# Kernel optimization log

Measured on AMD Instinct MI355X. Metric: run time of the kernel, lower is better.

## Reference

```python
import jax, jax.numpy as jnp
import numpy as np

B, S, DIM = 2, 2048, 2048
H, DH = 16, 128            # head_dim = dim // n_heads; decop_rot_dim == head_dim (required by the view)
LKV, LQ = 512, 1024        # latent kv / q compression dims


def setup_inputs() -> dict:
    key = jax.random.key(0)
    ks = jax.random.split(key, 12)
    w = lambda k, shape: jax.random.normal(k, shape, jnp.float32) * 0.02
    x = jax.random.normal(ks[0], (B, S, DIM), jnp.float32)
    # rotary table: angles[t, i] = t * 10000^(-2i/DH), complex passed as cos/sin pair
    inv_freq = 1.0 / (10000.0 ** (np.arange(0, DH, 2, dtype=np.float64) / DH))
    ang = np.outer(np.arange(S, dtype=np.float64), inv_freq)  # [S, DH/2]
    return {
        "x": x,
        "freq_cos": jnp.asarray(np.cos(ang), jnp.float32),
        "freq_sin": jnp.asarray(np.sin(ang), jnp.float32),
        "w_lq": w(ks[1], (LQ, DIM)),
        "w_lkv": w(ks[2], (LKV, DIM)),
        "w_q": w(ks[3], (H * DH, LQ)),
        "w_k": w(ks[4], (H * DH, LKV)),
        "w_v": w(ks[5], (H * DH, LKV)),
        "w_qr": w(ks[6], (H * DH, LQ)),
        "b_qr": w(ks[7], (H * DH,)),
        "w_kr": w(ks[8], (H * DH, DIM)),
        "b_kr": w(ks[9], (H * DH,)),
        "w_o": w(ks[10], (DIM, H * DH)),
        "b_o": w(ks[11], (DIM,)),
    }


def _rope(t, freq):
    # t: [B,S,H,DH]; freq: [S,DH/2] complex. Pairs (even,odd) along last dim rotated.
    b, s, h, d = t.shape
    tc = t.astype(jnp.float32).reshape(b, s, h, d // 2, 2)
    tc = jax.lax.complex(tc[..., 0], tc[..., 1]) * freq[None, :, None, :]
    return jnp.stack([jnp.real(tc), jnp.imag(tc)], axis=-1).reshape(b, s, h, d).astype(t.dtype)


def reference(x, freq_cos, freq_sin, w_lq, w_lkv, w_q, w_k, w_v, w_qr, b_qr, w_kr, b_kr, w_o, b_o):
    b, s, _ = x.shape
    freq = jax.lax.complex(freq_cos, freq_sin)          # [S, DH/2]
    cq = x @ w_lq.T                                      # [B,S,LQ]
    ckv = x @ w_lkv.T                                    # [B,S,LKV]
    q = (cq @ w_q.T).reshape(b, s, H, DH)
    qr = _rope((cq @ w_qr.T + b_qr).reshape(b, s, H, DH), freq)
    k = (ckv @ w_k.T).reshape(b, s, H, DH)
    kr = _rope((x @ w_kr.T + b_kr).reshape(b, s, H, DH), freq)
    v = (ckv @ w_v.T).reshape(b, s, H, DH)
    q = jnp.concatenate([q, qr], axis=-1)                # [B,S,H,2*DH]
    k = jnp.concatenate([k, kr], axis=-1)
    # note: scale uses sqrt(head_dim), NOT sqrt(2*head_dim), faithful to source
    scores = jnp.einsum('bqhd,bkhd->bhqk', q, k) / jnp.sqrt(jnp.float32(DH))
    att = jax.nn.softmax(scores.astype(jnp.float32), axis=-1).astype(q.dtype)
    out = jnp.einsum('bhqk,bkhd->bqhd', att, v).reshape(b, s, H * DH)
    return out @ w_o.T + b_o
```

## Files before the change

### kernel.cpp

```cpp
#include <hip/hip_runtime.h>
#include <hip/hip_bf16.h>


#define Bb 2
#define Ss 2048
#define DIMd 2048
#define Hh 16
#define DHd 128

typedef __hip_bfloat16 bf16;
typedef __attribute__((ext_vector_type(8))) short short8;
typedef __attribute__((ext_vector_type(4))) float floatx4;
typedef __attribute__((ext_vector_type(16))) float floatx16;
typedef __attribute__((ext_vector_type(2))) unsigned int uintx2;

#define MFMA(a, b, c) __builtin_amdgcn_mfma_f32_16x16x32_bf16((a), (b), (c), 0, 0, 0)
#define MFMA32(a, b, c) __builtin_amdgcn_mfma_f32_32x32x16_bf16((a), (b), (c), 0, 0, 0)

#define CEF (0.08838834764831845f * 1.4426950408889634f)

__device__ __forceinline__ void async16(const bf16* g, bf16* l) {
  __builtin_amdgcn_global_load_lds(
      (const __attribute__((address_space(1))) unsigned int*)g,
      (__attribute__((address_space(3))) unsigned int*)l, 16, 0, 0);
}

__global__ __launch_bounds__(256) void cvt_all(
    const float* x, const float* wlq, const float* wlkv, const float* wq,
    const float* wqr, const float* wk, const float* wv, const float* wkr,
    const float* wo, bf16* dx, bf16* dwlq, bf16* dwlkv, bf16* dwq, bf16* dwqr,
    bf16* dwk, bf16* dwv, bf16* dwkr, bf16* dwo) {
  long i = (long)blockIdx.x * 256 + threadIdx.x;
  const float* src;
  bf16* dst;
  long base;
  if (i < 2097152L)      { src = x;    dst = dx;    base = 0; }
  else if (i < 2621440L) { src = wlq;  dst = dwlq;  base = 2097152L; }
  else if (i < 2883584L) { src = wlkv; dst = dwlkv; base = 2621440L; }
  else if (i < 3407872L) { src = wq;   dst = dwq;   base = 2883584L; }
  else if (i < 3932160L) { src = wqr;  dst = dwqr;  base = 3407872L; }
  else if (i < 4194304L) { src = wk;   dst = dwk;   base = 3932160L; }
  else if (i < 4456448L) { src = wv;   dst = dwv;   base = 4194304L; }
  else if (i < 5505024L) { src = wkr;  dst = dwkr;  base = 4456448L; }
  else                   { src = wo;   dst = dwo;   base = 5505024L; }
  long j = i - base;
  float4 f = ((const float4*)src)[j];
  union { ushort4 u4; bf16 h[4]; } cv;
  cv.h[0] = __float2bfloat16(f.x);
  cv.h[1] = __float2bfloat16(f.y);
  cv.h[2] = __float2bfloat16(f.z);
  cv.h[3] = __float2bfloat16(f.w);
  ((ushort4*)dst)[j] = cv.u4;
}

template <int MODE>
__device__ __forceinline__ void gemm_body(const bf16* __restrict__ A,
                                          const bf16* __restrict__ Bw,
                                          const float* __restrict__ bias,
                                          void* __restrict__ Cout,
                                          void* __restrict__ Cout2,
                                          const float* __restrict__ fco,
                                          const float* __restrict__ fsi,
                                          int M, int N, int K, int lda) {
  extern __shared__ __align__(16) bf16 smem[];
  bf16* As = smem;
  bf16* Bs = smem + 8192;
  const int tid = threadIdx.x;
  const int lane = tid & 63;
  const int w = tid >> 6;
  const int wm = w & 1, wn = w >> 1;
  const int m0 = blockIdx.y * 128, n0 = blockIdx.x * 128;
  const int lr = lane & 15, lg = lane >> 4;

  floatx4 acc[4][4];
#pragma unroll
  for (int mi = 0; mi < 4; ++mi)
#pragma unroll
    for (int ni = 0; ni < 4; ++ni)
#pragma unroll
      for (int r = 0; r < 4; ++r) acc[mi][ni][r] = 0.f;

  for (int k0 = 0; k0 < K; k0 += 64) {
    __syncthreads();
#pragma unroll
    for (int i = 0; i < 4; ++i) {
      int c = i * 256 + tid;
      int row = c >> 3;
      int cg = (c & 7) ^ (row & 7);
      async16(A + (size_t)(m0 + row) * lda + k0 + cg * 8, As + (i * 256 + w * 64) * 8);
      async16(Bw + (size_t)(n0 + row) * K + k0 + cg * 8, Bs + (i * 256 + w * 64) * 8);
    }
    __syncthreads();

#pragma unroll
    for (int ks = 0; ks < 2; ++ks) {
      short8 af[4], bfr[4];
#pragma unroll
      for (int mi = 0; mi < 4; ++mi) {
        int row = wm * 64 + mi * 16 + lr;
        af[mi] = *(const short8*)&As[row * 64 + (((ks * 4 + lg) ^ (lr & 7)) * 8)];
      }
#pragma unroll
      for (int ni = 0; ni < 4; ++ni) {
        int row = wn * 64 + ni * 16 + lr;
        bfr[ni] = *(const short8*)&Bs[row * 64 + (((ks * 4 + lg) ^ (lr & 7)) * 8)];
      }
#pragma unroll
      for (int mi = 0; mi < 4; ++mi)
#pragma unroll
        for (int ni = 0; ni < 4; ++ni)
          acc[mi][ni] = MFMA(af[mi], bfr[ni], acc[mi][ni]);
    }
  }

  if (MODE == 5 && n0 >= 2048) {
    __syncthreads();
#pragma unroll
    for (int mi = 0; mi < 4; ++mi)
#pragma unroll
      for (int ni = 0; ni < 4; ++ni)
#pragma unroll
        for (int r = 0; r < 4; ++r) {
          int ml = wm * 64 + mi * 16 + lg * 4 + r;
          int nl = wn * 64 + ni * 16 + lr;
          smem[ml * 129 + nl] = __float2bfloat16(acc[mi][ni][r]);
        }
    __syncthreads();
    int bb = m0 >> 11, s0 = m0 & 2047;
    int hh = (n0 - 2048) >> 7;
    short* vbase = (short*)Cout2 + ((size_t)(bb * Hh + hh) * 128) * Ss;
#pragma unroll
    for (int pa = 0; pa < 8; ++pa) {
      int d = pa * 16 + (tid >> 4);
      int sc = (tid & 15) * 8;
      short8 v;
#pragma unroll
      for (int i = 0; i < 8; ++i) v[i] = *(const short*)&smem[(sc + i) * 129 + d];
      *(short8*)(vbase + (size_t)d * Ss + s0 + sc) = v;
    }
    return;
  }

#pragma unroll
  for (int mi = 0; mi < 4; ++mi)
#pragma unroll
    for (int ni = 0; ni < 4; ++ni)
#pragma unroll
      for (int r = 0; r < 4; ++r) {
        int m = m0 + wm * 64 + mi * 16 + lg * 4 + r;
        int n = n0 + wn * 64 + ni * 16 + lr;
        float v = acc[mi][ni][r];
        int bb = m >> 11, s = m & 2047;
        if (MODE == 3) {
          v += bias[n];
          ((float*)Cout)[(size_t)m * N + n] = v;
        } else if (MODE == 4) {
          if (n < 2048) {
            int hh = n >> 7, d = n & 127;
            ((bf16*)Cout)[((size_t)((bb * Hh + hh) * Ss + s)) * 256 + d] =
                __float2bfloat16(v * CEF);
          } else {
            int n2 = n - 2048;
            int hh = n2 >> 7, d = n2 & 127;
            v += bias[n2];
            float vp = __shfl_xor(v, 1, 64);
            float co = fco[s * 64 + (d >> 1)];
            float sn = fsi[s * 64 + (d >> 1)];
            v = (d & 1) ? (v * co + vp * sn) : (v * co - vp * sn);
            ((bf16*)Cout)[((size_t)((bb * Hh + hh) * Ss + s)) * 256 + 128 + d] =
                __float2bfloat16(v * CEF);
          }
        } else if (MODE == 5) {
          int hh = n >> 7, d = n & 127;
          ((bf16*)Cout)[((size_t)((bb * Hh + hh) * Ss + s)) * 256 + d] =
              __float2bfloat16(v);
        } else if (MODE == 6) {
          if (n < 1536) {
            ((bf16*)Cout)[(size_t)m * 1536 + n] = __float2bfloat16(v);
          } else {
            int n2 = n - 1536;
            int hh = n2 >> 7, d = n2 & 127;
            v += bias[n2];
            float vp = __shfl_xor(v, 1, 64);
            float co = fco[s * 64 + (d >> 1)];
            float sn = fsi[s * 64 + (d >> 1)];
            v = (d & 1) ? (v * co + vp * sn) : (v * co - vp * sn);
            ((bf16*)Cout2)[((size_t)((bb * Hh + hh) * Ss + s)) * 256 + 128 + d] =
                __float2bfloat16(v);
          }
        }
      }
}

template <int MODE>
__global__ __launch_bounds__(256, 4) void gemm_bt(const bf16* __restrict__ A,
                                                  const bf16* __restrict__ Bw,
                                                  const float* __restrict__ bias,
                                                  void* __restrict__ Cout,
                                                  void* __restrict__ Cout2,
                                                  const float* __restrict__ fco,
                                                  const float* __restrict__ fsi,
                                                  int M, int N, int K, int lda) {
  gemm_body<MODE>(A, Bw, bias, Cout, Cout2, fco, fsi, M, N, K, lda);
}

__global__ __launch_bounds__(256, 4) void gemm_qkv(const bf16* __restrict__ ccat,
                                                   const bf16* __restrict__ wqcat,
                                                   const bf16* __restrict__ wkvcat,
                                                   const float* __restrict__ bqr,
                                                   void* __restrict__ qcat,
                                                   void* __restrict__ kcat,
                                                   void* __restrict__ vt,
                                                   const float* __restrict__ fco,
                                                   const float* __restrict__ fsi) {
  if (blockIdx.z == 0)
    gemm_body<4>(ccat, wqcat, bqr, qcat, nullptr, fco, fsi, 4096, 4096, 1024, 1536);
  else
    gemm_body<5>(ccat + 1024, wkvcat, nullptr, kcat, vt, nullptr, nullptr, 4096, 4096, 512, 1536);
}

#define FA_STAGE(KSN, VSN, J)                                                    \
  {                                                                              \
    _Pragma("unroll") for (int i = 0; i < 4; ++i) {                              \
      int r = w * 8 + i * 2 + (lane >> 5);                                       \
      async16(Kb + (size_t)((J) + r) * 256 + (((lane & 31) ^ (r & 7)) * 8),      \
              KSN + (w * 8 + i * 2) * 256);                                      \
    }                                                                            \
    _Pragma("unroll") for (int i = 0; i < 2; ++i) {                              \
      int d = w * 32 + i * 16 + (lane >> 2);                                     \
      async16(Vb + (size_t)d * Ss + (J) + (((lane & 3) ^ ((d >> 1) & 3)) * 8),   \
              VSN + (w * 32 + i * 16) * 32);                                     \
    }                                                                            \
  }

#define FA_QKT(KP)                                                               \
  {                                                                              \
    _Pragma("unroll") for (int r = 0; r < 16; ++r) sf[r] = 0.f;                  \
    __builtin_amdgcn_s_setprio(1);                                               \
    _Pragma("unroll") for (int dt = 0; dt < 16; ++dt) {                          \
      short8 kf = *(const short8*)(KP[dt & 3] + (dt >> 2) * 64);                 \
      sf = MFMA32(kf, qf[dt], sf);                                               \
    }                                                                            \
    __builtin_amdgcn_s_setprio(0);                                               \
  }

#define FA_SM()                                                                  \
  {                                                                              \
    _Pragma("unroll") for (int rp = 0; rp < 8; ++rp) {                           \
      float p0 = exp2f(sf[2 * rp]);                                              \
      float p1 = exp2f(sf[2 * rp + 1]);                                          \
      l += p0 + p1;                                                              \
      bf16 b0 = __float2bfloat16(p0);                                            \
      bf16 b1 = __float2bfloat16(p1);                                            \
      pk[rp] = ((unsigned)*(const unsigned short*)&b1 << 16) |                   \
               *(const unsigned short*)&b0;                                      \
    }                                                                            \
  }

#define FA_PV(VQ)                                                                \
  {                                                                              \
    __builtin_amdgcn_s_setprio(1);                                               \
    _Pragma("unroll") for (int kb = 0; kb < 2; ++kb) {                           \
      uintx2 w02 = __builtin_amdgcn_permlane32_swap(pk[kb * 4 + 0],              \
                                                    pk[kb * 4 + 2], false, false); \
      uintx2 w13 = __builtin_amdgcn_permlane32_swap(pk[kb * 4 + 1],              \
                                                    pk[kb * 4 + 3], false, false); \
      union { unsigned u[4]; short8 s; } pa;                                     \
      pa.u[0] = w02.x; pa.u[1] = w13.x; pa.u[2] = w02.y; pa.u[3] = w13.y;        \
      _Pragma("unroll") for (int nb = 0; nb < 4; ++nb) {                         \
        short8 vf = *(const short8*)(VQ[kb] + nb * 1024);                        \
        oacc[nb] = MFMA32(pa.s, vf, oacc[nb]);                                   \
      }                                                                          \
    }                                                                            \
    __builtin_amdgcn_s_setprio(0);                                               \
  }

#define FA_BODY(VQpv, KPqk, KSst, VSst, Jst)                                     \
  FA_STAGE(KSst, VSst, Jst);                                                     \
  FA_PV(VQpv);                                                                   \
  asm volatile("s_waitcnt vmcnt(6)" ::: "memory");                               \
  __builtin_amdgcn_s_barrier();                                                  \
  FA_QKT(KPqk);                                                                  \
  FA_SM();

__global__ __launch_bounds__(256, 2) void flash_attn(const bf16* __restrict__ Q,
                                                     const bf16* __restrict__ Kc,
                                                     const bf16* __restrict__ Vt,
                                                     bf16* __restrict__ Oa) {
  __shared__ __align__(16) bf16 Ks0[32 * 256];
  __shared__ __align__(16) bf16 Ks1[32 * 256];
  __shared__ __align__(16) bf16 Ks2[32 * 256];
  __shared__ __align__(16) bf16 Vs0[128 * 32];
  __shared__ __align__(16) bf16 Vs1[128 * 32];
  __shared__ __align__(16) bf16 Vs2[128 * 32];

  const int lane = threadIdx.x & 63;
  const int w = threadIdx.x >> 6;
  const int m = lane & 31;
  const int hi = lane >> 5;
  const int bh = blockIdx.x;
  const int b = bh >> 4, h = bh & 15;
  const int q0 = blockIdx.y * 128 + w * 32;

  const bf16* Qb = Q + (size_t)bh * Ss * 256;
  const bf16* Kb = Kc + (size_t)bh * Ss * 256;
  const bf16* Vb = Vt + (size_t)bh * 128 * Ss;

  short8 qf[16];
  {
    const short* Qrow = (const short*)Qb + (size_t)(q0 + m) * 256 + hi * 8;
#pragma unroll
    for (int dt = 0; dt < 16; ++dt) qf[dt] = *(const short8*)(Qrow + dt * 16);
  }

  const int key = m & 7;
  const int vkey = (m >> 1) & 3;
  const short *kp0[4], *kp1[4], *kp2[4];
#pragma unroll
  for (int dl = 0; dl < 4; ++dl) {
    int off = m * 256 + (((2 * dl + hi) ^ key) * 8);
    kp0[dl] = (const short*)Ks0 + off;
    kp1[dl] = (const short*)Ks1 + off;
    kp2[dl] = (const short*)Ks2 + off;
  }
  const short *vq0[2], *vq1[2], *vq2[2];
#pragma unroll
  for (int kb = 0; kb < 2; ++kb) {
    int off = m * 32 + (((2 * kb + hi) ^ vkey) * 8);
    vq0[kb] = (const short*)Vs0 + off;
    vq1[kb] = (const short*)Vs1 + off;
    vq2[kb] = (const short*)Vs2 + off;
  }

  float l = 0.f;
  floatx16 sf;
  unsigned pk[8];
  floatx16 oacc[4];
#pragma unroll
  for (int nb = 0; nb < 4; ++nb)
#pragma unroll
    for (int r = 0; r < 16; ++r) oacc[nb][r] = 0.f;

  FA_STAGE(Ks0, Vs0, 0);
  FA_STAGE(Ks1, Vs1, 32);
  asm volatile("s_waitcnt vmcnt(6)" ::: "memory");
  __builtin_amdgcn_s_barrier();
  FA_QKT(kp0);
  FA_SM();

#pragma unroll 1
  for (int c = 0; c < 20; ++c) {
    const int j2 = (3 * c + 2) * 32;
    FA_BODY(vq0, kp1, Ks2, Vs2, j2);
    FA_BODY(vq1, kp2, Ks0, Vs0, j2 + 32);
    FA_BODY(vq2, kp0, Ks1, Vs1, j2 + 64);
  }
  FA_BODY(vq0, kp1, Ks2, Vs2, 62 * 32);
  FA_BODY(vq1, kp2, Ks0, Vs0, 63 * 32);
  FA_PV(vq2);
  asm volatile("s_waitcnt vmcnt(0)" ::: "memory");
  __builtin_amdgcn_s_barrier();
  FA_QKT(kp0);
  FA_SM();
  FA_PV(vq0);

  float lsum = l + __shfl_xor(l, 32, 64);
  float inv = 1.f / lsum;

#pragma unroll
  for (int r = 0; r < 16; ++r) {
    int qr = (r & 3) + 8 * (r >> 2) + 4 * hi;
    float invr = __shfl(inv, (lane & 32) + qr, 64);
    int s = q0 + qr;
#pragma unroll
    for (int nb = 0; nb < 4; ++nb) {
      int d = nb * 32 + m;
      Oa[((size_t)(b * Ss + s)) * (Hh * 128) + h * 128 + d] =
          __float2bfloat16(oacc[nb][r] * invr);
    }
  }
}

extern "C" void kernel_launch(void* const* d_in, const int* in_sizes, int n_in,
                              void* d_out, int out_size, void* d_ws, size_t ws_size,
                              hipStream_t stream) {
  const float* x    = (const float*)d_in[0];
  const float* fco  = (const float*)d_in[1];
  const float* fsi  = (const float*)d_in[2];
  const float* wlq  = (const float*)d_in[3];
  const float* wlkv = (const float*)d_in[4];
  const float* wq   = (const float*)d_in[5];
  const float* wk   = (const float*)d_in[6];
  const float* wv   = (const float*)d_in[7];
  const float* wqr  = (const float*)d_in[8];
  const float* bqr  = (const float*)d_in[9];
  const float* wkr  = (const float*)d_in[10];
  const float* bkr  = (const float*)d_in[11];
  const float* wo   = (const float*)d_in[12];
  const float* bo   = (const float*)d_in[13];

  char* ws = (char*)d_ws;
  size_t o = 0;
  bf16* x_b    = (bf16*)(ws + o); o += (size_t)Bb * Ss * DIMd * 2;
  bf16* wbig   = (bf16*)(ws + o); o += (size_t)3584 * 2048 * 2;
  bf16* wqcat  = (bf16*)(ws + o); o += (size_t)4096 * 1024 * 2;
  bf16* wkvcat = (bf16*)(ws + o); o += (size_t)4096 * 512 * 2;
  bf16* wo_b   = (bf16*)(ws + o); o += (size_t)2048 * 2048 * 2;
  bf16* ccat   = (bf16*)(ws + o); o += (size_t)4096 * 1536 * 2;
  bf16* qcat   = (bf16*)(ws + o); o += (size_t)Bb * Hh * Ss * 256 * 2;
  bf16* kcat   = (bf16*)(ws + o); o += (size_t)Bb * Hh * Ss * 256 * 2;
  bf16* vt     = (bf16*)(ws + o); o += (size_t)Bb * Hh * 128 * Ss * 2;
  bf16* attn   = (bf16*)(ws + o); o += (size_t)4096 * 2048 * 2;

  cvt_all<<<25600, 256, 0, stream>>>(
      x, wlq, wlkv, wq, wqr, wk, wv, wkr, wo,
      x_b,
      wbig,
      wbig + (size_t)1024 * 2048,
      wqcat,
      wqcat + (size_t)2048 * 1024,
      wkvcat,
      wkvcat + (size_t)2048 * 512,
      wbig + (size_t)1536 * 2048,
      wo_b);

  const int M = Bb * Ss;
  const int GEMM_LDS = 128 * 129 * 2;
  gemm_bt<6><<<dim3(28, 32), 256, GEMM_LDS, stream>>>(
      x_b, wbig, bkr, ccat, kcat, fco, fsi, M, 3584, 2048, 2048);
  gemm_qkv<<<dim3(32, 32, 2), 256, GEMM_LDS, stream>>>(
      ccat, wqcat, wkvcat, bqr, qcat, kcat, vt, fco, fsi);

  flash_attn<<<dim3(Bb * Hh, Ss / 128), 256, 0, stream>>>(qcat, kcat, vt, attn);

  gemm_bt<3><<<dim3(16, 32), 256, GEMM_LDS, stream>>>(
      attn, wo_b, bo, (float*)d_out, nullptr, nullptr, nullptr, M, 2048, 2048, 2048);
}
```

Baseline: 454.5 us.

## Add 256x256-tile double-buffered GEMM for latent and Q projections

Adds a new 512-thread GEMM kernel with 256x256 output tiles, 128KB of double-buffered LDS loaded asynchronously with XOR swizzling, and MFMA priority hints. It is used for the x→latent/kr projection and the Q/QR projection. The K/V projection is split back into its own launch of the old 128-tile kernel. The goal is more data reuse per tile and better overlap of loads with MFMA work. In exchange, occupancy drops, the latent GEMM grid becomes small (224 blocks), and the fused QKV launch turns into two launches.

```diff
diff --git a/kernel.cpp b/kernel.cpp
--- a/kernel.cpp
+++ b/kernel.cpp
@@ -154,7 +154,120 @@
         if (MODE == 3) {
           v += bias[n];
           ((float*)Cout)[(size_t)m * N + n] = v;
-        } else if (MODE == 4) {
+        } else if (MODE == 5) {
+          int hh = n >> 7, d = n & 127;
+          ((bf16*)Cout)[((size_t)((bb * Hh + hh) * Ss + s)) * 256 + d] =
+              __float2bfloat16(v);
+        }
+      }
+}
+
+template <int MODE>
+__global__ __launch_bounds__(256, 4) void gemm_bt(const bf16* __restrict__ A,
+                                                  const bf16* __restrict__ Bw,
+                                                  const float* __restrict__ bias,
+                                                  void* __restrict__ Cout,
+                                                  void* __restrict__ Cout2,
+                                                  const float* __restrict__ fco,
+                                                  const float* __restrict__ fsi,
+                                                  int M, int N, int K, int lda) {
+  gemm_body<MODE>(A, Bw, bias, Cout, Cout2, fco, fsi, M, N, K, lda);
+}
+
+#define G2_STAGE(BUF, TT)                                                      \
+  {                                                                            \
+    bf16* db = smem + (BUF) * 32768;                                           \
+    _Pragma("unroll") for (int i = 0; i < 4; ++i) {                            \
+      int c = i * 512 + tid;                                                   \
+      int row = c >> 3;                                                        \
+      int cg = (c & 7) ^ (row & 7);                                            \
+      async16(A + (size_t)(m0 + row) * lda + (TT) * 64 + cg * 8,               \
+              db + (i * 512 + w * 64) * 8);                                    \
+    }                                                                          \
+    _Pragma("unroll") for (int i = 0; i < 4; ++i) {                            \
+      int c = i * 512 + tid;                                                   \
+      int row = c >> 3;                                                        \
+      int cg = (c & 7) ^ (row & 7);                                            \
+      async16(Bw + (size_t)(n0 + row) * KTOT + (TT) * 64 + cg * 8,             \
+              db + 16384 + (i * 512 + w * 64) * 8);                            \
+    }                                                                          \
+  }
+
+#define G2_COMPUTE(BUF)                                                        \
+  {                                                                            \
+    const bf16* cb = smem + (BUF) * 32768;                                     \
+    _Pragma("unroll") for (int ks = 0; ks < 2; ++ks) {                         \
+      short8 af[8], bq[4];                                                     \
+      _Pragma("unroll") for (int mi = 0; mi < 8; ++mi) {                       \
+        int row = wm * 128 + mi * 16 + lr;                                     \
+        af[mi] = *(const short8*)&cb[row * 64 + (((ks * 4 + lg) ^ (lr & 7)) * 8)]; \
+      }                                                                        \
+      _Pragma("unroll") for (int ni = 0; ni < 4; ++ni) {                       \
+        int row = wn * 64 + ni * 16 + lr;                                      \
+        bq[ni] = *(const short8*)&cb[16384 + row * 64 +                        \
+                                     (((ks * 4 + lg) ^ (lr & 7)) * 8)];        \
+      }                                                                        \
+      __builtin_amdgcn_s_setprio(1);                                           \
+      _Pragma("unroll") for (int mi = 0; mi < 8; ++mi)                         \
+        _Pragma("unroll") for (int ni = 0; ni < 4; ++ni)                       \
+            acc[mi][ni] = MFMA(af[mi], bq[ni], acc[mi][ni]);                   \
+      __builtin_amdgcn_s_setprio(0);                                           \
+    }                                                                          \
+  }
+
+template <int MODE, int KTOT>
+__global__ __launch_bounds__(512, 2) void gemm256(const bf16* __restrict__ A,
+                                                  const bf16* __restrict__ Bw,
+                                                  const float* __restrict__ bias,
+                                                  void* __restrict__ Cout,
+                                                  void* __restrict__ Cout2,
+                                                  const float* __restrict__ fco,
+                                                  const float* __restrict__ fsi,
+                                                  int M, int N, int lda) {
+  extern __shared__ __align__(16) bf16 smem[];
+  constexpr int NT = KTOT / 64;
+  const int tid = threadIdx.x;
+  const int lane = tid & 63;
+  const int w = tid >> 6;
+  const int wm = w >> 2, wn = w & 3;
+  const int m0 = blockIdx.y * 256, n0 = blockIdx.x * 256;
+  const int lr = lane & 15, lg = lane >> 4;
+
+  floatx4 acc[8][4];
+#pragma unroll
+  for (int mi = 0; mi < 8; ++mi)
+#pragma unroll
+    for (int ni = 0; ni < 4; ++ni)
+#pragma unroll
+      for (int r = 0; r < 4; ++r) acc[mi][ni][r] = 0.f;
+
+  G2_STAGE(0, 0);
+  asm volatile("s_waitcnt vmcnt(0)" ::: "memory");
+  __builtin_amdgcn_s_barrier();
+
+#pragma unroll 1
+  for (int t = 0; t < NT; t += 2) {
+    G2_STAGE(1, t + 1);
+    G2_COMPUTE(0);
+    asm volatile("s_waitcnt vmcnt(0)" ::: "memory");
+    __builtin_amdgcn_s_barrier();
+    if (t + 2 < NT) G2_STAGE(0, t + 2);
+    G2_COMPUTE(1);
+    asm volatile("s_waitcnt vmcnt(0)" ::: "memory");
+    __builtin_amdgcn_s_barrier();
+  }
+
+#pragma unroll
+  for (int mi = 0; mi < 8; ++mi)
+#pragma unroll
+    for (int ni = 0; ni < 4; ++ni)
+#pragma unroll
+      for (int r = 0; r < 4; ++r) {
+        int m = m0 + wm * 128 + mi * 16 + lg * 4 + r;
+        int n = n0 + wn * 64 + ni * 16 + lr;
+        float v = acc[mi][ni][r];
+        int bb = m >> 11, s = m & 2047;
+        if (MODE == 4) {
           if (n < 2048) {
             int hh = n >> 7, d = n & 127;
             ((bf16*)Cout)[((size_t)((bb * Hh + hh) * Ss + s)) * 256 + d] =
@@ -170,10 +283,6 @@
             ((bf16*)Cout)[((size_t)((bb * Hh + hh) * Ss + s)) * 256 + 128 + d] =
                 __float2bfloat16(v * CEF);
           }
-        } else if (MODE == 5) {
-          int hh = n >> 7, d = n & 127;
-          ((bf16*)Cout)[((size_t)((bb * Hh + hh) * Ss + s)) * 256 + d] =
-              __float2bfloat16(v);
         } else if (MODE == 6) {
           if (n < 1536) {
             ((bf16*)Cout)[(size_t)m * 1536 + n] = __float2bfloat16(v);
@@ -190,33 +299,6 @@
           }
         }
       }
-}
-
-template <int MODE>
-__global__ __launch_bounds__(256, 4) void gemm_bt(const bf16* __restrict__ A,
-                                                  const bf16* __restrict__ Bw,
-                                                  const float* __restrict__ bias,
-                                                  void* __restrict__ Cout,
-                                                  void* __restrict__ Cout2,
-                                                  const float* __restrict__ fco,
-                                                  const float* __restrict__ fsi,
-                                                  int M, int N, int K, int lda) {
-  gemm_body<MODE>(A, Bw, bias, Cout, Cout2, fco, fsi, M, N, K, lda);
-}
-
-__global__ __launch_bounds__(256, 4) void gemm_qkv(const bf16* __restrict__ ccat,
-                                                   const bf16* __restrict__ wqcat,
-                                                   const bf16* __restrict__ wkvcat,
-                                                   const float* __restrict__ bqr,
-                                                   void* __restrict__ qcat,
-                                                   void* __restrict__ kcat,
-                                                   void* __restrict__ vt,
-                                                   const float* __restrict__ fco,
-                                                   const float* __restrict__ fsi) {
-  if (blockIdx.z == 0)
-    gemm_body<4>(ccat, wqcat, bqr, qcat, nullptr, fco, fsi, 4096, 4096, 1024, 1536);
-  else
-    gemm_body<5>(ccat + 1024, wkvcat, nullptr, kcat, vt, nullptr, nullptr, 4096, 4096, 512, 1536);
 }
 
 #define FA_STAGE(KSN, VSN, J)                                                    \
@@ -412,6 +494,15 @@
   bf16* vt     = (bf16*)(ws + o); o += (size_t)Bb * Hh * 128 * Ss * 2;
   bf16* attn   = (bf16*)(ws + o); o += (size_t)4096 * 2048 * 2;
 
+  static bool g2init = false;
+  if (!g2init) {
+    hipFuncSetAttribute(reinterpret_cast<const void*>(gemm256<6, 2048>),
+                        hipFuncAttributeMaxDynamicSharedMemorySize, 131072);
+    hipFuncSetAttribute(reinterpret_cast<const void*>(gemm256<4, 1024>),
+                        hipFuncAttributeMaxDynamicSharedMemorySize, 131072);
+    g2init = true;
+  }
+
   cvt_all<<<25600, 256, 0, stream>>>(
       x, wlq, wlkv, wq, wqr, wk, wv, wkr, wo,
       x_b,
@@ -426,10 +517,13 @@
 
   const int M = Bb * Ss;
   const int GEMM_LDS = 128 * 129 * 2;
-  gemm_bt<6><<<dim3(28, 32), 256, GEMM_LDS, stream>>>(
-      x_b, wbig, bkr, ccat, kcat, fco, fsi, M, 3584, 2048, 2048);
-  gemm_qkv<<<dim3(32, 32, 2), 256, GEMM_LDS, stream>>>(
-      ccat, wqcat, wkvcat, bqr, qcat, kcat, vt, fco, fsi);
+
+  gemm256<6, 2048><<<dim3(14, 16), 512, 131072, stream>>>(
+      x_b, wbig, bkr, ccat, kcat, fco, fsi, M, 3584, 2048);
+  gemm256<4, 1024><<<dim3(16, 16), 512, 131072, stream>>>(
+      ccat, wqcat, bqr, qcat, nullptr, fco, fsi, M, 4096, 1536);
+  gemm_bt<5><<<dim3(32, 32), 256, GEMM_LDS, stream>>>(
+      ccat + 1024, wkvcat, nullptr, kcat, vt, nullptr, nullptr, M, 4096, 512, 1536);
 
   flash_attn<<<dim3(Bb * Hh, Ss / 128), 256, 0, stream>>>(qcat, kcat, vt, attn);
 
```

After: 550.3 us. 1.21x slower.
